# Kernel tuning notes

Measured on AMD Instinct MI355X. Metric: run time of the kernel, lower is better.

Reference implementation:

```python
import jax, jax.numpy as jnp
import numpy as np

B, T = 1024, 512
BN_EPS = 1e-5


def _lstm_dir(x, w_ih, w_hh, b, reverse=False):
    """Single-direction LSTM, PyTorch gate order (i, f, g, o).
    x: [B, T, D]; w_ih: [4H, D]; w_hh: [4H, H]; b: [4H]. Returns [B, T, H]."""
    if reverse:
        x = x[:, ::-1]
    xw = jnp.einsum('btd,gd->btg', x, w_ih) + b  # precompute input contribution [B,T,4H]
    H = w_hh.shape[1]
    h0 = jnp.zeros((x.shape[0], H), x.dtype)

    def step(carry, xw_t):
        h, c = carry
        g = xw_t + h @ w_hh.T
        i, f, gg, o = jnp.split(g, 4, axis=-1)
        c = jax.nn.sigmoid(f) * c + jax.nn.sigmoid(i) * jnp.tanh(gg)
        h = jax.nn.sigmoid(o) * jnp.tanh(c)
        return (h, c), h

    _, ys = jax.lax.scan(step, (h0, h0), jnp.swapaxes(xw, 0, 1))
    ys = jnp.swapaxes(ys, 0, 1)  # [B,T,H]
    if reverse:
        ys = ys[:, ::-1]
    return ys


def _bilstm(x, w_ih, w_hh, b):
    # w_ih: [2,4H,D] (dir 0 = forward, dir 1 = backward)
    return jnp.concatenate([
        _lstm_dir(x, w_ih[0], w_hh[0], b[0]),
        _lstm_dir(x, w_ih[1], w_hh[1], b[1], reverse=True),
    ], axis=-1)


def _pool2(x):
    # MaxPool1d(2) over time on channel-last layout: [B,T,C] -> [B,T//2,C]
    b, t, c = x.shape
    return x.reshape(b, t // 2, 2, c).max(axis=2)


def setup_inputs() -> dict:
    key = jax.random.key(0)
    ks = iter(jax.random.split(key, 32))
    s = 0.1  # small init to avoid gate saturation
    d = {}
    d['x'] = jax.random.normal(next(ks), (B, 11, T), jnp.float32)
    d['conv_w'] = jax.random.normal(next(ks), (64, 11), jnp.float32) * s
    d['conv_b'] = jax.random.normal(next(ks), (64,), jnp.float32) * s
    d['bn_gamma'] = jax.random.uniform(next(ks), (64,), jnp.float32, 0.5, 1.5)
    d['bn_beta'] = jax.random.normal(next(ks), (64,), jnp.float32) * s
    d['bn_mean'] = jax.random.normal(next(ks), (64,), jnp.float32) * s
    d['bn_var'] = jax.random.uniform(next(ks), (64,), jnp.float32, 0.5, 1.5)
    for name, shp in [
        ('l1_wih0', (2, 64, 64)), ('l1_whh0', (2, 64, 16)), ('l1_b0', (2, 64)),
        ('l1_wih1', (2, 64, 32)), ('l1_whh1', (2, 64, 16)), ('l1_b1', (2, 64)),
        ('l2_wih0', (2, 32, 32)), ('l2_whh0', (2, 32, 8)), ('l2_b0', (2, 32)),
        ('l2_wih1', (2, 32, 16)), ('l2_whh1', (2, 32, 8)), ('l2_b1', (2, 32)),
        ('l3_wih0', (2, 16, 16)), ('l3_whh0', (2, 16, 4)), ('l3_b0', (2, 16)),
    ]:
        d[name] = jax.random.normal(next(ks), shp, jnp.float32) * s
    return d


def reference(x, conv_w, conv_b, bn_gamma, bn_beta, bn_mean, bn_var,
              l1_wih0, l1_whh0, l1_b0, l1_wih1, l1_whh1, l1_b1,
              l2_wih0, l2_whh0, l2_b0, l2_wih1, l2_whh1, l2_b1,
              l3_wih0, l3_whh0, l3_b0):
    # conv1x1: [B,11,T] -> [B,64,T]
    y = jnp.einsum('bct,oc->bot', x, conv_w) + conv_b[:, None]
    # BatchNorm1d (inference, running stats), fused scale/shift
    inv = bn_gamma / jnp.sqrt(bn_var + BN_EPS)
    y = (y - bn_mean[:, None]) * inv[:, None] + bn_beta[:, None]
    y = jnp.swapaxes(y, 1, 2)                      # [B,T,64]
    y = _bilstm(y, l1_wih0, l1_whh0, l1_b0)        # [B,T,32]
    y = _bilstm(y, l1_wih1, l1_whh1, l1_b1)        # [B,T,32]
    y = _pool2(y)                                  # [B,T/2,32]
    y = _bilstm(y, l2_wih0, l2_whh0, l2_b0)        # [B,T/2,16]
    y = _bilstm(y, l2_wih1, l2_whh1, l2_b1)        # [B,T/2,16]
    y = _pool2(y)                                  # [B,T/4,16]
    y = _bilstm(y, l3_wih0, l3_whh0, l3_b0)        # [B,T/4,8]
    return jnp.swapaxes(y, 1, 2)                   # [B,8,T/4]
```

## Files before the change

kernel.cpp:

```cpp
#include <hip/hip_runtime.h>

#define TB 128

typedef float v2f __attribute__((ext_vector_type(2)));
typedef _Float16 f16;
typedef _Float16 h2v __attribute__((ext_vector_type(2)));

__device__ __forceinline__ float rcp_f(float x) { return __builtin_amdgcn_rcpf(x); }
__device__ __forceinline__ float exp2_f(float x) { return __builtin_amdgcn_exp2f(x); }
__device__ __forceinline__ float dpp_xor2(float x) {
  return __int_as_float(__builtin_amdgcn_update_dpp(0, __float_as_int(x), 0x4E, 0xF, 0xF, true));
}
__device__ __forceinline__ float dpp_xor1(float x) {
  return __int_as_float(__builtin_amdgcn_update_dpp(0, __float_as_int(x), 0xB1, 0xF, 0xF, true));
}

#if __has_builtin(__builtin_amdgcn_fdot2)
__device__ __forceinline__ float fdot2(h2v a, h2v b, float c) {
  return __builtin_amdgcn_fdot2(a, b, c, false);
}
#else
__device__ __forceinline__ float fdot2(h2v a, h2v b, float c) {
  return fmaf((float)a.x, (float)b.x, fmaf((float)a.y, (float)b.y, c));
}
#endif

template<int D, int H, int T, int INS, int OUTS, int DEPTH, bool HIN,
         bool POOL, bool TOUT, typename OutT, typename InT>
__device__ __forceinline__ void scan(const void* wv, const float* hr,
                                     float bb, float am, float ab,
                                     const InT* in, OutT* out,
                                     int dir, int wl, float* h_base) {
  constexpr int NF4 = HIN ? (D / 8) : (D / 4);
  constexpr int NH4 = H / 4;
  const int tau = wl & 3;
  const int j = (wl >> 2) & (H - 1);
  const bool st = (tau == 1) && ((wl >> 2) < H);
  if (wl < H) h_base[wl] = 0.f;
  __builtin_amdgcn_wave_barrier();
  float4 hreg[NH4];
#pragma unroll
  for (int i = 0; i < NH4; ++i) hreg[i] = *(const float4*)(h_base + 4 * i);
  __builtin_amdgcn_wave_barrier();

  int t = dir ? (T - 1) : 0;
  const int dt = dir ? -1 : 1;

  float4 bufs[DEPTH][NF4];
  auto ldin = [&](float4* dst, int tt) {
    tt = tt < 0 ? 0 : (tt > T - 1 ? T - 1 : tt);
    const float4* p = (const float4*)((const char*)in + (size_t)tt * INS * sizeof(InT));
#pragma unroll
    for (int i = 0; i < NF4; ++i) dst[i] = p[i];
  };
  auto xwdot = [&](const float4* b) -> float {
    if constexpr (HIN) {
      const h2v* hp = (const h2v*)b;
      const h2v* wh = (const h2v*)wv;
      float a0 = bb, a1 = 0.f, a2 = 0.f, a3 = 0.f;
#pragma unroll
      for (int i = 0; i < D / 2; i += 4) {
        a0 = fdot2(wh[i + 0], hp[i + 0], a0);
        a1 = fdot2(wh[i + 1], hp[i + 1], a1);
        a2 = fdot2(wh[i + 2], hp[i + 2], a2);
        a3 = fdot2(wh[i + 3], hp[i + 3], a3);
      }
      return (a0 + a1) + (a2 + a3);
    } else {
      const float* c = (const float*)b;
      const float* wr = (const float*)wv;
      v2f q0 = {bb, 0.f}, q1 = {0.f, 0.f};
#pragma unroll
      for (int i = 0; i < D; i += 4) {
        q0 = __builtin_elementwise_fma(*(const v2f*)(wr + i), *(const v2f*)(c + i), q0);
        q1 = __builtin_elementwise_fma(*(const v2f*)(wr + i + 2), *(const v2f*)(c + i + 2), q1);
      }
      v2f qs = q0 + q1;
      return qs.x + qs.y;
    }
  };

#pragma unroll
  for (int k = 0; k < DEPTH; ++k) ldin(bufs[k], t + k * dt);
  float xw = xwdot(bufs[0]);
  float cs = 0.f, pm = 0.f;

  for (int s = 0; s < T; s += DEPTH) {
#pragma unroll
    for (int k = 0; k < DEPTH; ++k) {
      v2f r0 = {xw, 0.f}, r1 = {0.f, 0.f};
#pragma unroll
      for (int i = 0; i < NH4; ++i) {
        r0 = __builtin_elementwise_fma(*(const v2f*)(hr + 4 * i), (v2f){hreg[i].x, hreg[i].y}, r0);
        r1 = __builtin_elementwise_fma(*(const v2f*)(hr + 4 * i + 2), (v2f){hreg[i].z, hreg[i].w}, r1);
      }
      v2f rs = r0 + r1;
      float acc = rs.x + rs.y;
      float sg = rcp_f(1.f + exp2_f(-acc));
      float a = fmaf(am, sg, ab);
      float b = dpp_xor2(a);
      float p = a * b;
      float q = dpp_xor1(p);
      float fv = (tau == 1) ? a : b;
      float ov = (tau == 1) ? b : a;
      cs = fmaf(fv, cs, q);
      float th = fmaf(2.f, rcp_f(1.f + exp2_f(-2.8853900818f * cs)), -1.f);
      float hv = ov * th;
      if (st) h_base[j] = hv;
      __builtin_amdgcn_wave_barrier();
#pragma unroll
      for (int i = 0; i < NH4; ++i) hreg[i] = *(const float4*)(h_base + 4 * i);
      xw = xwdot(bufs[(k + 1) % DEPTH]);
      ldin(bufs[k], t + DEPTH * dt);
      if (st) {
        if constexpr (TOUT) {
          out[(dir * H + j) * T + t] = (OutT)hv;
        } else if constexpr (POOL) {
          if (k & 1) out[(t >> 1) * OUTS + dir * H + j] = (OutT)fmaxf(pm, hv);
          else pm = hv;
        } else {
          out[t * OUTS + dir * H + j] = (OutT)hv;
        }
      }
      __builtin_amdgcn_wave_barrier();
      t += dt;
    }
  }
}

template<int D, int H>
__device__ __forceinline__ void load_wbh(const float* __restrict__ wih,
                                         const float* __restrict__ whh,
                                         const float* __restrict__ bias,
                                         int dir, int wl,
                                         h2v* wh, float* hr, float& bb,
                                         float& am, float& ab) {
  constexpr float L2E = 1.4426950408889634f;
  const int tau = wl & 3;
  const int j = (wl >> 2) & (H - 1);
  const bool isg = (tau == 2);
  const float k = isg ? 2.f * L2E : L2E;
  am = isg ? 2.f : 1.f;
  ab = isg ? -1.f : 0.f;
  const int row = dir * 4 * H + tau * H + j;
  const float* p = wih + row * D;
#pragma unroll
  for (int i = 0; i < D / 2; ++i)
    wh[i] = (h2v){(f16)(p[2 * i] * k), (f16)(p[2 * i + 1] * k)};
  const float* q = whh + row * H;
#pragma unroll
  for (int i = 0; i < H; ++i) hr[i] = q[i] * k;
  bb = bias[row] * k;
}

__global__ __launch_bounds__(TB) void lstm_all(
    const float* __restrict__ x,
    const float* __restrict__ conv_w, const float* __restrict__ conv_b,
    const float* __restrict__ bn_g, const float* __restrict__ bn_b,
    const float* __restrict__ bn_m, const float* __restrict__ bn_v,
    const float* __restrict__ w1a_ih, const float* __restrict__ w1a_hh, const float* __restrict__ b1a,
    const float* __restrict__ w1b_ih, const float* __restrict__ w1b_hh, const float* __restrict__ b1b,
    const float* __restrict__ w2a_ih, const float* __restrict__ w2a_hh, const float* __restrict__ b2a,
    const float* __restrict__ w2b_ih, const float* __restrict__ w2b_hh, const float* __restrict__ b2b,
    const float* __restrict__ w3_ih, const float* __restrict__ w3_hh, const float* __restrict__ b3,
    float* __restrict__ out, f16* __restrict__ ws, int row0) {
  const int row = row0 + blockIdx.x;
  const int tid = threadIdx.x;
  const int wave = tid >> 6;
  const int lane = tid & 63;

  __shared__ __align__(16) char R1[24576];
  __shared__ __align__(16) f16 A2h[256 * 16];
  __shared__ __align__(16) float w2c[64][11];
  __shared__ float b2c[64];
  __shared__ __align__(16) float hb[32];

  float (*xs)[12] = (float(*)[12])R1;
  f16* LBh = (f16*)R1;
  f16* LB2h = (f16*)(R1 + 16384);
  f16* Ah = ws + (size_t)blockIdx.x * 16384;

  const float* xrow = x + (size_t)row * 5632;
  for (int i = tid; i < 5632; i += TB) {
    int c = i >> 9, t = i & 511;
    xs[t][c] = xrow[i];
  }
  for (int i = tid; i < 512; i += TB) xs[i][11] = 0.f;
  if (tid < 64) {
    float inv = bn_g[tid] * rsqrtf(bn_v[tid] + 1e-5f);
    for (int c = 0; c < 11; ++c) w2c[tid][c] = conv_w[tid * 11 + c] * inv;
    b2c[tid] = fmaf(conv_b[tid] - bn_m[tid], inv, bn_b[tid]);
  }
  __syncthreads();

  {
    constexpr float L2E = 1.4426950408889634f;
    const int tau = lane & 3;
    const int j = lane >> 2;
    const int row_l = wave * 64 + tau * 16 + j;
    float weff[12], beff;
#pragma unroll
    for (int c = 0; c < 12; ++c) weff[c] = 0.f;
    const float* wih = w1a_ih + row_l * 64;
    beff = b1a[row_l];
    for (int d = 0; d < 64; ++d) {
      float wd = wih[d];
      beff = fmaf(wd, b2c[d], beff);
#pragma unroll
      for (int c = 0; c < 11; ++c) weff[c] = fmaf(wd, w2c[d][c], weff[c]);
    }
    const bool isg = (tau == 2);
    const float k = isg ? 2.f * L2E : L2E;
#pragma unroll
    for (int c = 0; c < 12; ++c) weff[c] *= k;
    beff *= k;
    float am = isg ? 2.f : 1.f, ab = isg ? -1.f : 0.f;
    float hrw[16];
    const float* q = w1a_hh + row_l * 16;
#pragma unroll
    for (int i = 0; i < 16; ++i) hrw[i] = q[i] * k;
    scan<12, 16, 512, 12, 32, 2, false, false, false, f16, float>(
        weff, hrw, beff, am, ab, &xs[0][0], Ah, wave, lane, hb + wave * 16);
  }
  __syncthreads();

  {
    h2v wh[16]; float hr[16], bb, am, ab;
    load_wbh<32, 16>(w1b_ih, w1b_hh, b1b, wave, lane, wh, hr, bb, am, ab);
    scan<32, 16, 512, 32, 32, 4, true, true, false, f16, f16>(
        wh, hr, bb, am, ab, Ah, LBh, wave, lane, hb + wave * 16);
  }
  __syncthreads();

  if (wave == 0) {
    const int dir = lane >> 5, wl = lane & 31;
    h2v wh[16]; float hr[8], bb, am, ab;
    load_wbh<32, 8>(w2a_ih, w2a_hh, b2a, dir, wl, wh, hr, bb, am, ab);
    scan<32, 8, 256, 32, 16, 2, true, false, false, f16, f16>(
        wh, hr, bb, am, ab, LBh, A2h, dir, wl, hb + dir * 16);
  }
  __syncthreads();

  if (wave == 0) {
    const int dir = lane >> 5, wl = lane & 31;
    h2v wh[8]; float hr[8], bb, am, ab;
    load_wbh<16, 8>(w2b_ih, w2b_hh, b2b, dir, wl, wh, hr, bb, am, ab);
    scan<16, 8, 256, 16, 16, 2, true, true, false, f16, f16>(
        wh, hr, bb, am, ab, A2h, LB2h, dir, wl, hb + dir * 16);
  }
  __syncthreads();

  if (wave == 0) {
    const int dir = lane >> 5, wl = lane & 31;
    h2v wh[8]; float hr[4], bb, am, ab;
    load_wbh<16, 4>(w3_ih, w3_hh, b3, dir, wl, wh, hr, bb, am, ab);
    scan<16, 4, 128, 16, 8, 2, true, false, true, float, f16>(
        wh, hr, bb, am, ab, LB2h, out + (size_t)row * 1024, dir, wl, hb + dir * 16);
  }
}

extern "C" void kernel_launch(void* const* d_in, const int* in_sizes, int n_in,
                              void* d_out, int out_size, void* d_ws, size_t ws_size,
                              hipStream_t stream) {
  const float* x      = (const float*)d_in[0];
  const float* conv_w = (const float*)d_in[1];
  const float* conv_b = (const float*)d_in[2];
  const float* bn_g   = (const float*)d_in[3];
  const float* bn_b   = (const float*)d_in[4];
  const float* bn_m   = (const float*)d_in[5];
  const float* bn_v   = (const float*)d_in[6];
  const float* w1a_ih = (const float*)d_in[7];
  const float* w1a_hh = (const float*)d_in[8];
  const float* b1a    = (const float*)d_in[9];
  const float* w1b_ih = (const float*)d_in[10];
  const float* w1b_hh = (const float*)d_in[11];
  const float* b1b    = (const float*)d_in[12];
  const float* w2a_ih = (const float*)d_in[13];
  const float* w2a_hh = (const float*)d_in[14];
  const float* b2a    = (const float*)d_in[15];
  const float* w2b_ih = (const float*)d_in[16];
  const float* w2b_hh = (const float*)d_in[17];
  const float* b2b    = (const float*)d_in[18];
  const float* w3_ih  = (const float*)d_in[19];
  const float* w3_hh  = (const float*)d_in[20];
  const float* b3     = (const float*)d_in[21];

  const size_t per_row_bytes = 16384 * sizeof(f16);
  int rows_per = (int)(ws_size / per_row_bytes);
  if (rows_per < 1) rows_per = 1;
  if (rows_per > 1024) rows_per = 1024;

  for (int r0 = 0; r0 < 1024; r0 += rows_per) {
    int n = 1024 - r0;
    if (n > rows_per) n = rows_per;
    lstm_all<<<n, TB, 0, stream>>>(x, conv_w, conv_b, bn_g, bn_b, bn_m, bn_v,
                                   w1a_ih, w1a_hh, b1a, w1b_ih, w1b_hh, b1b,
                                   w2a_ih, w2a_hh, b2a, w2b_ih, w2b_hh, b2b,
                                   w3_ih, w3_hh, b3,
                                   (float*)d_out, (f16*)d_ws, r0);
  }
}
```

Measured before the change: 379.8 us.

## Exchange hidden state via DPP/permlane cross-lane ops instead of LDS in small layers

For the layer-2 and layer-3 LSTMs, the recurrent hidden state is now gathered across lanes with DPP row broadcasts and permlane16 swaps, replacing writes and reads through shared memory with wave barriers. The recurrent weights are permuted at load time to match the gathered lane order, and the gate nonlinearity is rearranged to handle all four tau positions without the earlier broadcast. The g-gate affine constants are also changed so the tanh scale folds into am/ab, which removes one multiply per step on the cell tanh. The intent is to shorten the serial per-timestep latency. The cost is more complex lane-selection logic and a correctness dependence on the DPP and permlane lane mapping.

After: 404.6 us. 1.07x slower.

```diff
diff --git a/kernel.cpp b/kernel.cpp
--- a/kernel.cpp
+++ b/kernel.cpp
@@ -8,11 +8,46 @@
 
 __device__ __forceinline__ float rcp_f(float x) { return __builtin_amdgcn_rcpf(x); }
 __device__ __forceinline__ float exp2_f(float x) { return __builtin_amdgcn_exp2f(x); }
-__device__ __forceinline__ float dpp_xor2(float x) {
-  return __int_as_float(__builtin_amdgcn_update_dpp(0, __float_as_int(x), 0x4E, 0xF, 0xF, true));
-}
-__device__ __forceinline__ float dpp_xor1(float x) {
-  return __int_as_float(__builtin_amdgcn_update_dpp(0, __float_as_int(x), 0xB1, 0xF, 0xF, true));
+
+template<int CTRL>
+__device__ __forceinline__ float dpp_f(float x) {
+  return __int_as_float(__builtin_amdgcn_update_dpp(0, __float_as_int(x), CTRL, 0xF, 0xF, true));
+}
+__device__ __forceinline__ float dpp_xor2(float x) { return dpp_f<0x4E>(x); }
+__device__ __forceinline__ float dpp_xor1(float x) { return dpp_f<0xB1>(x); }
+
+__device__ __forceinline__ void xchg16(float x, float& lo, float& hi) {
+#if __has_builtin(__builtin_amdgcn_permlane16_swap)
+  auto r = __builtin_amdgcn_permlane16_swap(__float_as_uint(x), __float_as_uint(x), false, false);
+  lo = __uint_as_float(r[0]);
+  hi = __uint_as_float(r[1]);
+#else
+  lo = x;
+  hi = __int_as_float(__builtin_amdgcn_ds_swizzle(__float_as_int(x), 0x401F));
+#endif
+}
+
+template<int H>
+__device__ __forceinline__ void gather_h(float x, float* g) {
+  float a0 = x;
+  float a1 = dpp_f<0x124>(x);
+  float a2 = dpp_f<0x128>(x);
+  float a3 = dpp_f<0x12C>(x);
+  if constexpr (H == 4) {
+    g[0] = a0; g[1] = a1; g[2] = a2; g[3] = a3;
+  } else {
+    xchg16(a0, g[0], g[1]); xchg16(a1, g[2], g[3]);
+    xchg16(a2, g[4], g[5]); xchg16(a3, g[6], g[7]);
+  }
+}
+
+template<int H>
+__device__ __forceinline__ void calib_w(const float* __restrict__ whh_row,
+                                        float k, int j, float* wp) {
+  float g[H];
+  gather_h<H>((float)j, g);
+#pragma unroll
+  for (int m = 0; m < H; ++m) wp[m] = whh_row[(int)g[m]] * k;
 }
 
 #if __has_builtin(__builtin_amdgcn_fdot2)
@@ -24,6 +59,9 @@
   return fmaf((float)a.x, (float)b.x, fmaf((float)a.y, (float)b.y, c));
 }
 #endif
+
+#define AM_G (-5.7707801636f)
+#define AB_G (2.8853900818f)
 
 template<int D, int H, int T, int INS, int OUTS, int DEPTH, bool HIN,
          bool POOL, bool TOUT, typename OutT, typename InT>
@@ -104,7 +142,7 @@
       float fv = (tau == 1) ? a : b;
       float ov = (tau == 1) ? b : a;
       cs = fmaf(fv, cs, q);
-      float th = fmaf(2.f, rcp_f(1.f + exp2_f(-2.8853900818f * cs)), -1.f);
+      float th = fmaf(2.f, rcp_f(1.f + exp2_f(cs)), -1.f);
       float hv = ov * th;
       if (st) h_base[j] = hv;
       __builtin_amdgcn_wave_barrier();
@@ -128,6 +166,90 @@
   }
 }
 
+template<int D, int H, int T, int INS, int OUTS, int DEPTH,
+         bool POOL, bool TOUT, typename OutT>
+__device__ __forceinline__ void scan_gx(const h2v* wh, const float* wp,
+                                        float bb, float am, float ab,
+                                        const f16* in, OutT* out,
+                                        int dir, int wl) {
+  constexpr int NF4 = D / 8;
+  const int tau = wl & 3;
+  const int j = (wl >> 2) & (H - 1);
+  const bool st = (tau == 1) && ((wl >> 2) < H);
+  const bool t1 = (tau & 1) != 0;
+  const bool t2 = (tau & 2) != 0;
+
+  int t = dir ? (T - 1) : 0;
+  const int dt = dir ? -1 : 1;
+
+  float4 bufs[DEPTH][NF4];
+  auto ldin = [&](float4* dst, int tt) {
+    tt = tt < 0 ? 0 : (tt > T - 1 ? T - 1 : tt);
+    const float4* p = (const float4*)((const char*)in + (size_t)tt * INS * sizeof(f16));
+#pragma unroll
+    for (int i = 0; i < NF4; ++i) dst[i] = p[i];
+  };
+  auto xwdot = [&](const float4* b) -> float {
+    const h2v* hp = (const h2v*)b;
+    float a0 = bb, a1 = 0.f, a2 = 0.f, a3 = 0.f;
+#pragma unroll
+    for (int i = 0; i < D / 2; i += 4) {
+      a0 = fdot2(wh[i + 0], hp[i + 0], a0);
+      a1 = fdot2(wh[i + 1], hp[i + 1], a1);
+      a2 = fdot2(wh[i + 2], hp[i + 2], a2);
+      a3 = fdot2(wh[i + 3], hp[i + 3], a3);
+    }
+    return (a0 + a1) + (a2 + a3);
+  };
+
+#pragma unroll
+  for (int k = 0; k < DEPTH; ++k) ldin(bufs[k], t + k * dt);
+  float xw = xwdot(bufs[0]);
+  float hprev = 0.f, cs = 0.f, pm = 0.f;
+
+  for (int s = 0; s < T; s += DEPTH) {
+#pragma unroll
+    for (int k = 0; k < DEPTH; ++k) {
+      float g[H];
+      gather_h<H>(hprev, g);
+      float a0 = xw, a1 = 0.f;
+#pragma unroll
+      for (int m = 0; m < H; m += 4) {
+        a0 = fmaf(wp[m + 0], g[m + 0], a0);
+        a1 = fmaf(wp[m + 1], g[m + 1], a1);
+        a0 = fmaf(wp[m + 2], g[m + 2], a0);
+        a1 = fmaf(wp[m + 3], g[m + 3], a1);
+      }
+      float acc = a0 + a1;
+      float sg = rcp_f(1.f + exp2_f(-acc));
+      float a = fmaf(am, sg, ab);
+      float b = dpp_xor2(a);
+      float e = dpp_xor1(a);
+      float d = dpp_xor1(b);
+      float ig = t1 ? e * d : a * b;
+      float fv = t1 ? (t2 ? b : a) : (t2 ? d : e);
+      float ov = t1 ? (t2 ? a : b) : (t2 ? e : d);
+      cs = fmaf(fv, cs, ig);
+      float th = fmaf(2.f, rcp_f(1.f + exp2_f(cs)), -1.f);
+      float hv = ov * th;
+      hprev = hv;
+      xw = xwdot(bufs[(k + 1) % DEPTH]);
+      ldin(bufs[k], t + DEPTH * dt);
+      if (st) {
+        if constexpr (TOUT) {
+          out[(dir * H + j) * T + t] = (OutT)hv;
+        } else if constexpr (POOL) {
+          if (k & 1) out[(t >> 1) * OUTS + dir * H + j] = (OutT)fmaxf(pm, hv);
+          else pm = hv;
+        } else {
+          out[t * OUTS + dir * H + j] = (OutT)hv;
+        }
+      }
+      t += dt;
+    }
+  }
+}
+
 template<int D, int H>
 __device__ __forceinline__ void load_wbh(const float* __restrict__ wih,
                                          const float* __restrict__ whh,
@@ -140,8 +262,8 @@
   const int j = (wl >> 2) & (H - 1);
   const bool isg = (tau == 2);
   const float k = isg ? 2.f * L2E : L2E;
-  am = isg ? 2.f : 1.f;
-  ab = isg ? -1.f : 0.f;
+  am = isg ? AM_G : 1.f;
+  ab = isg ? AB_G : 0.f;
   const int row = dir * 4 * H + tau * H + j;
   const float* p = wih + row * D;
 #pragma unroll
@@ -150,6 +272,29 @@
   const float* q = whh + row * H;
 #pragma unroll
   for (int i = 0; i < H; ++i) hr[i] = q[i] * k;
+  bb = bias[row] * k;
+}
+
+template<int D, int H>
+__device__ __forceinline__ void load_wbg(const float* __restrict__ wih,
+                                         const float* __restrict__ whh,
+                                         const float* __restrict__ bias,
+                                         int dir, int wl,
+                                         h2v* wh, float* wp, float& bb,
+                                         float& am, float& ab) {
+  constexpr float L2E = 1.4426950408889634f;
+  const int tau = wl & 3;
+  const int j = (wl >> 2) & (H - 1);
+  const bool isg = (tau == 2);
+  const float k = isg ? 2.f * L2E : L2E;
+  am = isg ? AM_G : 1.f;
+  ab = isg ? AB_G : 0.f;
+  const int row = dir * 4 * H + tau * H + j;
+  const float* p = wih + row * D;
+#pragma unroll
+  for (int i = 0; i < D / 2; ++i)
+    wh[i] = (h2v){(f16)(p[2 * i] * k), (f16)(p[2 * i + 1] * k)};
+  calib_w<H>(whh + row * H, k, j, wp);
   bb = bias[row] * k;
 }
 
@@ -214,7 +359,7 @@
 #pragma unroll
     for (int c = 0; c < 12; ++c) weff[c] *= k;
     beff *= k;
-    float am = isg ? 2.f : 1.f, ab = isg ? -1.f : 0.f;
+    float am = isg ? AM_G : 1.f, ab = isg ? AB_G : 0.f;
     float hrw[16];
     const float* q = w1a_hh + row_l * 16;
 #pragma unroll
@@ -234,28 +379,28 @@
 
   if (wave == 0) {
     const int dir = lane >> 5, wl = lane & 31;
-    h2v wh[16]; float hr[8], bb, am, ab;
-    load_wbh<32, 8>(w2a_ih, w2a_hh, b2a, dir, wl, wh, hr, bb, am, ab);
-    scan<32, 8, 256, 32, 16, 2, true, false, false, f16, f16>(
-        wh, hr, bb, am, ab, LBh, A2h, dir, wl, hb + dir * 16);
+    h2v wh[16]; float wp[8], bb, am, ab;
+    load_wbg<32, 8>(w2a_ih, w2a_hh, b2a, dir, wl, wh, wp, bb, am, ab);
+    scan_gx<32, 8, 256, 32, 16, 2, false, false, f16>(
+        wh, wp, bb, am, ab, LBh, A2h, dir, wl);
   }
   __syncthreads();
 
   if (wave == 0) {
     const int dir = lane >> 5, wl = lane & 31;
-    h2v wh[8]; float hr[8], bb, am, ab;
-    load_wbh<16, 8>(w2b_ih, w2b_hh, b2b, dir, wl, wh, hr, bb, am, ab);
-    scan<16, 8, 256, 16, 16, 2, true, true, false, f16, f16>(
-        wh, hr, bb, am, ab, A2h, LB2h, dir, wl, hb + dir * 16);
+    h2v wh[8]; float wp[8], bb, am, ab;
+    load_wbg<16, 8>(w2b_ih, w2b_hh, b2b, dir, wl, wh, wp, bb, am, ab);
+    scan_gx<16, 8, 256, 16, 16, 2, true, false, f16>(
+        wh, wp, bb, am, ab, A2h, LB2h, dir, wl);
   }
   __syncthreads();
 
   if (wave == 0) {
     const int dir = lane >> 5, wl = lane & 31;
-    h2v wh[8]; float hr[4], bb, am, ab;
-    load_wbh<16, 4>(w3_ih, w3_hh, b3, dir, wl, wh, hr, bb, am, ab);
-    scan<16, 4, 128, 16, 8, 2, true, false, true, float, f16>(
-        wh, hr, bb, am, ab, LB2h, out + (size_t)row * 1024, dir, wl, hb + dir * 16);
+    h2v wh[8]; float wp[4], bb, am, ab;
+    load_wbg<16, 4>(w3_ih, w3_hh, b3, dir, wl, wh, wp, bb, am, ab);
+    scan_gx<16, 4, 128, 16, 8, 2, false, true, float>(
+        wh, wp, bb, am, ab, LB2h, out + (size_t)row * 1024, dir, wl);
   }
 }
 
```
